# Performance work log

Measured on AMD Instinct MI355X. Metric: run time of the kernel, lower is better.

## Reference

```python
import jax, jax.numpy as jnp
import numpy as np

B, S, HID = 1, 2048, 2048   # batch, block_size, hidden_dim
H, D = 16, 128              # num_heads, head_dim
WORLD_SIZE = 4
LOCAL_BLOCK_IDX = 3         # last rank: all kv blocks are causally visible


def setup_inputs() -> dict:
    key = jax.random.key(0)
    ks = jax.random.split(key, 5)
    w = lambda k: jax.random.normal(k, (H * D, HID), dtype=jnp.float32) * 0.02
    return {
        "hidden_states": jax.random.normal(ks[0], (B, S, HID), dtype=jnp.float32),
        "q_w": w(ks[1]), "q_b": jnp.zeros((H * D,), jnp.float32),
        "k_w": w(ks[2]), "k_b": jnp.zeros((H * D,), jnp.float32),
        "v_w": w(ks[3]), "v_b": jnp.zeros((H * D,), jnp.float32),
        "o_w": jax.random.normal(ks[4], (HID, H * D), dtype=jnp.float32) * 0.02,
        "o_b": jnp.zeros((HID,), jnp.float32),
        "world_size": WORLD_SIZE,
        "local_block_idx": LOCAL_BLOCK_IDX,
    }


def reference(hidden_states, q_w, q_b, k_w, k_b, v_w, v_b, o_w, o_b,
              world_size, local_block_idx):
    Bsz, Sq, _ = hidden_states.shape

    def proj(w, b):  # (B,S,HID) -> (B,H,S,D)
        return (hidden_states @ w.T + b).reshape(Bsz, Sq, H, D).transpose(0, 2, 1, 3)

    q, k, v = proj(q_w, q_b), proj(k_w, k_b), proj(v_w, v_b)
    scale = D ** -0.5

    # ring_send_recv is a local copy, so K/V are identical every ring step;
    # only the causal masking differs (triu mask on the diagonal block step).
    scores_base = jnp.einsum('bhqd,bhkd->bhqk', q, k) * scale
    tri = jnp.triu(jnp.ones((Sq, Sq), bool), k=1)
    scores_diag = jnp.where(tri, -jnp.inf, scores_base)

    out = jnp.zeros((Bsz, H, Sq, D), hidden_states.dtype)
    mx = jnp.full((Bsz, H, Sq, 1), -jnp.inf, hidden_states.dtype)
    se = jnp.zeros((Bsz, H, Sq, 1), hidden_states.dtype)

    for step in range(world_size):  # small fixed ring loop
        kv_idx = (local_block_idx - step) % world_size
        scores = scores_diag if kv_idx == local_block_idx else scores_base
        # OnlineSoftmax.update (faithful, including block-wise normalization)
        bm = scores.max(axis=-1, keepdims=True)
        nm = jnp.maximum(mx, bm)
        old_s = jnp.exp(mx - nm)
        new_s = jnp.exp(bm - nm)
        be = jnp.exp(scores - bm)
        bs = be.sum(axis=-1, keepdims=True)
        se = se * old_s + bs * new_s
        aw = be / (bs + 1e-8)
        bo = jnp.einsum('bhqk,bhkd->bhqd', aw, v)
        out = out * old_s + bo * new_s
        mx = nm

    out = out / (se + 1e-8)  # OnlineSoftmax.finalize
    out = out.transpose(0, 2, 1, 3).reshape(Bsz, Sq, H * D)
    return out @ o_w.T + o_b
```

## Files before the change

kernel.cpp:

```cpp
#include <hip/hip_runtime.h>
#include <hip/hip_bf16.h>
#include <stdint.h>
#include <stddef.h>


typedef __attribute__((ext_vector_type(8))) short bf16x8;
typedef __attribute__((ext_vector_type(4))) float f32x4;

#define MFMA_BF16(a, b, c) __builtin_amdgcn_mfma_f32_16x16x32_bf16((a), (b), (c), 0, 0, 0)

__device__ __forceinline__ void load16_lds(const void* g, void* l) {
  __builtin_amdgcn_global_load_lds((const __attribute__((address_space(1))) void*)g,
                                   (__attribute__((address_space(3))) void*)l,
                                   16, 0, 0);
}

__device__ __forceinline__ unsigned short f2bf(float x) {
  union { __hip_bfloat16 b; unsigned short u; } cv;
  cv.b = __float2bfloat16(x);
  return cv.u;
}

__global__ __launch_bounds__(256) void cvt_all(
    const float4* __restrict__ s0, const float4* __restrict__ s1,
    const float4* __restrict__ s2, const float4* __restrict__ s3,
    const float4* __restrict__ s4,
    ushort4* __restrict__ d0, ushort4* __restrict__ d1,
    ushort4* __restrict__ d2, ushort4* __restrict__ d3,
    ushort4* __restrict__ d4) {
  const int seg = blockIdx.x >> 12;
  const int i = ((blockIdx.x & 4095) << 8) + threadIdx.x;
  const float4* s = seg == 0 ? s0 : seg == 1 ? s1 : seg == 2 ? s2 : seg == 3 ? s3 : s4;
  ushort4* d = seg == 0 ? d0 : seg == 1 ? d1 : seg == 2 ? d2 : seg == 3 ? d3 : d4;
  float4 v = s[i];
  ushort4 o;
  o.x = f2bf(v.x); o.y = f2bf(v.y); o.z = f2bf(v.z); o.w = f2bf(v.w);
  d[i] = o;
}

__global__ __launch_bounds__(256) void gemm_qkv(
    const unsigned short* __restrict__ A, const unsigned short* __restrict__ Bt,
    const float* __restrict__ qb, const float* __restrict__ kb,
    const float* __restrict__ vb,
    unsigned short* __restrict__ Qo, unsigned short* __restrict__ Ko,
    unsigned short* __restrict__ Vt) {
  __shared__ __align__(16) unsigned short sA[128 * 64];
  __shared__ __align__(16) unsigned short sB[128 * 64];
  const int tid = threadIdx.x;
  const int wave = tid >> 6, lane = tid & 63;
  const int quad = lane >> 4, l16 = lane & 15;
  const int wr = wave >> 1, wc = wave & 1;
  const int m0 = blockIdx.y << 7, n0 = blockIdx.x << 7;

  f32x4 acc[4][4] = {};

  for (int k0 = 0; k0 < 2048; k0 += 64) {
    __syncthreads();
#pragma unroll
    for (int t = 0; t < 4; t++) {
      const int i = t * 4 + wave;
      const int idx = i * 64 + lane;
      const int row = idx >> 3;
      const int c = (idx & 7) ^ (row & 7);
      load16_lds(A + (size_t)(m0 + row) * 2048 + k0 + c * 8, &sA[i * 512]);
      load16_lds(Bt + (size_t)(n0 + row) * 2048 + k0 + c * 8, &sB[i * 512]);
    }
    __syncthreads();
#pragma unroll
    for (int ks = 0; ks < 2; ks++) {
      bf16x8 af[4], bfr[4];
#pragma unroll
      for (int i = 0; i < 4; i++) {
        const int cs = ((ks * 4 + quad) ^ (l16 & 7)) << 3;
        af[i] = *(const bf16x8*)&sA[(wr * 64 + i * 16 + l16) * 64 + cs];
        bfr[i] = *(const bf16x8*)&sB[(wc * 64 + i * 16 + l16) * 64 + cs];
      }
#pragma unroll
      for (int mi = 0; mi < 4; mi++)
#pragma unroll
        for (int ni = 0; ni < 4; ni++)
          acc[mi][ni] = MFMA_BF16(af[mi], bfr[ni], acc[mi][ni]);
    }
  }

  const float qscale = 0.088388347648318447f * 1.4426950408889634f;
#pragma unroll
  for (int mi = 0; mi < 4; mi++) {
    const int row = m0 + wr * 64 + mi * 16 + quad * 4;
#pragma unroll
    for (int ni = 0; ni < 4; ni++) {
      const int col = n0 + wc * 64 + ni * 16 + l16;
#pragma unroll
      for (int r = 0; r < 4; r++) {
        const float v = acc[mi][ni][r];
        const int rr = row + r;
        if (col < 2048) {
          const int hh = col >> 7, d = col & 127;
          Qo[((size_t)hh * 2048 + rr) * 128 + d] = f2bf((v + qb[col]) * qscale);
        } else if (col < 4096) {
          const int f = col - 2048;
          const int hh = f >> 7, d = f & 127;
          Ko[((size_t)hh * 2048 + rr) * 128 + d] = f2bf(v + kb[f]);
        } else {
          const int f = col - 4096;
          const int hh = f >> 7, d = f & 127;
          Vt[((size_t)hh * 128 + d) * 2048 + rr] = f2bf(v + vb[f]);
        }
      }
    }
  }
}

__global__ __launch_bounds__(256, 2) void attn_fwd(
    const unsigned short* __restrict__ Q, const unsigned short* __restrict__ K,
    const unsigned short* __restrict__ V,
    unsigned short* __restrict__ O,
    const int* __restrict__ wsp) {
  const int qt = blockIdx.x, h = blockIdx.y;
  const int tid = threadIdx.x;
  const int wave = tid >> 6, lane = tid & 63;
  const int quad = lane >> 4, l16 = lane & 15;

  __shared__ __align__(16) unsigned short sK0[64 * 128];
  __shared__ __align__(16) unsigned short sK1[64 * 128];
  __shared__ __align__(16) unsigned short sV0[128 * 64];
  __shared__ __align__(16) unsigned short sV1[128 * 64];
  __shared__ __align__(16) unsigned short sP[4][16 * 64];

  const unsigned short* Qh = Q + (size_t)h * 2048 * 128;
  const unsigned short* Kh = K + (size_t)h * 2048 * 128;
  const unsigned short* Vh = V + (size_t)h * 128 * 2048;
  unsigned short* sPw = sP[wave];

  for (int c = wave; c < 16; c += 4) {
    const int rowc = lane >> 4;
    const int row = c * 4 + rowc;
    const int blk = (lane & 15) ^ (row & 15);
    load16_lds(Qh + (size_t)(qt * 64 + row) * 128 + blk * 8, &sK0[c * 512]);
  }
  __syncthreads();

  bf16x8 qf[4];
#pragma unroll
  for (int ds = 0; ds < 4; ds++)
    qf[ds] = *(const bf16x8*)&sK0[(wave * 16 + l16) * 128 + (((ds * 4 + quad) ^ l16) << 3)];
  __syncthreads();

  float m1 = -3.0e38f, l1 = 0.f, m2 = -3.0e38f, l2 = 0.f;
  f32x4 o1[8], o2[8];
#pragma unroll
  for (int j = 0; j < 8; j++) { o1[j] = f32x4{0.f, 0.f, 0.f, 0.f}; o2[j] = f32x4{0.f, 0.f, 0.f, 0.f}; }

  auto stageKV = [&](int kt, unsigned short* kDst, unsigned short* vDst) {
    const int k0 = kt << 6;
    for (int c = wave; c < 16; c += 4) {
      {
        const int rowc = lane >> 4;
        const int row = c * 4 + rowc;
        const int blk = (lane & 15) ^ (row & 15);
        load16_lds(Kh + (size_t)(k0 + row) * 128 + blk * 8, &kDst[c * 512]);
      }
      {
        const int rowc = lane >> 3;
        const int row = c * 8 + rowc;
        const int blk = (lane & 7) ^ (rowc & 7);
        load16_lds(Vh + (size_t)row * 2048 + k0 + blk * 8, &vDst[c * 512]);
      }
    }
  };

  auto softmax_update = [&](float& m, float& l, f32x4 (&o)[8],
                            const f32x4 (&stt)[4], bool masked, int k0) {
    const int qg = qt * 64 + wave * 16 + l16;
    float t[4][4];
    float mx = -3.0e38f;
#pragma unroll
    for (int ni = 0; ni < 4; ni++)
#pragma unroll
      for (int r = 0; r < 4; r++) {
        float v = stt[ni][r];
        if (masked && (k0 + ni * 16 + quad * 4 + r > qg)) v = -3.0e38f;
        t[ni][r] = v;
        mx = fmaxf(mx, v);
      }
    mx = fmaxf(mx, __shfl_xor(mx, 16));
    mx = fmaxf(mx, __shfl_xor(mx, 32));
    const float mn = fmaxf(m, mx);
    const float al = exp2f(m - mn);
    float rs = 0.f;
#pragma unroll
    for (int ni = 0; ni < 4; ni++) {
      union { unsigned short u[4]; uint2 v; } pk;
#pragma unroll
      for (int r = 0; r < 4; r++) {
        const float p = exp2f(t[ni][r] - mn);
        rs += p;
        pk.u[r] = f2bf(p);
      }
      const int off =
          l16 * 64 + (((ni * 2 + (quad >> 1)) ^ (l16 & 7)) << 3) + ((quad & 1) << 2);
      *(uint2*)&sPw[off] = pk.v;
    }
    rs += __shfl_xor(rs, 16);
    rs += __shfl_xor(rs, 32);
    const bool grew = !__all(mn == m);
    l = l * al + rs;
    m = mn;
    if (grew) {
#pragma unroll
      for (int r = 0; r < 4; r++) {
        const int src = (lane & 48) + quad * 4 + r;
        const float ab = __shfl(al, src);
#pragma unroll
        for (int j = 0; j < 8; j++) o[j][r] *= ab;
      }
    }
  };

  auto pv = [&](f32x4 (&o)[8], const unsigned short* vBuf) {
#pragma unroll
    for (int ks = 0; ks < 2; ks++) {
      const int cs = (((ks * 4 + quad) ^ (l16 & 7)) << 3);
      const bf16x8 pf = *(const bf16x8*)&sPw[l16 * 64 + cs];
#pragma unroll
      for (int j = 0; j < 8; j++) {
        const bf16x8 vf = *(const bf16x8*)&vBuf[(j * 16 + l16) * 64 + cs];
        o[j] = MFMA_BF16(pf, vf, o[j]);
      }
    }
  };

  auto compute_tile = [&](int kt, const unsigned short* kBuf,
                          const unsigned short* vBuf) {
    const int k0 = kt << 6;
    f32x4 st[4];
#pragma unroll
    for (int ni = 0; ni < 4; ni++) st[ni] = f32x4{0.f, 0.f, 0.f, 0.f};
#pragma unroll
    for (int ds = 0; ds < 4; ds++) {
#pragma unroll
      for (int ni = 0; ni < 4; ni++) {
        const bf16x8 kf =
            *(const bf16x8*)&kBuf[(ni * 16 + l16) * 128 + (((ds * 4 + quad) ^ l16) << 3)];
        st[ni] = MFMA_BF16(kf, qf[ds], st[ni]);
      }
    }

    if (kt == qt) {
      m1 = m2; l1 = l2;
#pragma unroll
      for (int j = 0; j < 8; j++) o1[j] = o2[j];
      softmax_update(m1, l1, o1, st, true, k0);
      pv(o1, vBuf);
    }
    softmax_update(m2, l2, o2, st, false, k0);
    pv(o2, vBuf);
  };

  stageKV(0, sK0, sV0);
  for (int kt2 = 0; kt2 < 32; kt2 += 2) {
    __syncthreads();
    if (kt2 + 1 < 32) stageKV(kt2 + 1, sK1, sV1);
    compute_tile(kt2, sK0, sV0);
    __syncthreads();
    if (kt2 + 2 < 32) stageKV(kt2 + 2, sK0, sV0);
    compute_tile(kt2 + 1, sK1, sV1);
  }

  const float fws = (float)(wsp[0] - 1);
  const float a = exp2f(m1 - m2);
  const float se = l1 * a + fws * l2;
  const float inv = 1.0f / (se + 1e-8f);
  const float f1 = (a / (l1 + 1e-8f)) * inv;
  const float f2 = (fws / (l2 + 1e-8f)) * inv;
#pragma unroll
  for (int r = 0; r < 4; r++) {
    const int src = (lane & 48) + quad * 4 + r;
    const float f1b = __shfl(f1, src);
    const float f2b = __shfl(f2, src);
    const int row = qt * 64 + wave * 16 + quad * 4 + r;
#pragma unroll
    for (int j = 0; j < 8; j++) {
      const float ov = o1[j][r] * f1b + o2[j][r] * f2b;
      O[(size_t)row * 2048 + h * 128 + j * 16 + l16] = f2bf(ov);
    }
  }
}

__global__ __launch_bounds__(256) void gemm_o(
    const unsigned short* __restrict__ A, const unsigned short* __restrict__ Bt,
    const float* __restrict__ ob, float* __restrict__ Cout) {
  __shared__ __align__(16) unsigned short sA[64 * 128];
  __shared__ __align__(16) unsigned short sB[128 * 128];
  const int tid = threadIdx.x;
  const int wave = tid >> 6, lane = tid & 63;
  const int quad = lane >> 4, l16 = lane & 15;
  const int wm = wave >> 1, wn = wave & 1;
  const int m0 = blockIdx.y << 6, n0 = blockIdx.x << 7;

  f32x4 acc[2][4] = {};

  for (int k0 = 0; k0 < 2048; k0 += 128) {
    __syncthreads();
#pragma unroll
    for (int t = 0; t < 4; t++) {
      const int i = t * 4 + wave;
      const int idx = i * 64 + lane;
      const int row = idx >> 4;
      const int c = (idx & 15) ^ (row & 15);
      load16_lds(A + (size_t)(m0 + row) * 2048 + k0 + c * 8, &sA[i * 512]);
    }
#pragma unroll
    for (int t = 0; t < 8; t++) {
      const int i = t * 4 + wave;
      const int idx = i * 64 + lane;
      const int row = idx >> 4;
      const int c = (idx & 15) ^ (row & 15);
      load16_lds(Bt + (size_t)(n0 + row) * 2048 + k0 + c * 8, &sB[i * 512]);
    }
    __syncthreads();
#pragma unroll
    for (int ks = 0; ks < 4; ks++) {
      const int cs = ((ks * 4 + quad) ^ l16) << 3;
      bf16x8 af[2], bfr[4];
#pragma unroll
      for (int i = 0; i < 2; i++)
        af[i] = *(const bf16x8*)&sA[(wm * 32 + i * 16 + l16) * 128 + cs];
#pragma unroll
      for (int i = 0; i < 4; i++)
        bfr[i] = *(const bf16x8*)&sB[(wn * 64 + i * 16 + l16) * 128 + cs];
#pragma unroll
      for (int mi = 0; mi < 2; mi++)
#pragma unroll
        for (int ni = 0; ni < 4; ni++)
          acc[mi][ni] = MFMA_BF16(af[mi], bfr[ni], acc[mi][ni]);
    }
  }

#pragma unroll
  for (int mi = 0; mi < 2; mi++) {
    const int row = m0 + wm * 32 + mi * 16 + quad * 4;
#pragma unroll
    for (int ni = 0; ni < 4; ni++) {
      const int col = n0 + wn * 64 + ni * 16 + l16;
#pragma unroll
      for (int r = 0; r < 4; r++) {
        Cout[(size_t)(row + r) * 2048 + col] = acc[mi][ni][r] + ob[col];
      }
    }
  }
}

extern "C" void kernel_launch(void* const* d_in, const int* in_sizes, int n_in,
                              void* d_out, int out_size, void* d_ws, size_t ws_size,
                              hipStream_t stream) {
  (void)in_sizes; (void)n_in; (void)out_size; (void)ws_size;
  const float* hs = (const float*)d_in[0];
  const float* qw = (const float*)d_in[1];
  const float* qb = (const float*)d_in[2];
  const float* kw = (const float*)d_in[3];
  const float* kb = (const float*)d_in[4];
  const float* vw = (const float*)d_in[5];
  const float* vb = (const float*)d_in[6];
  const float* ow = (const float*)d_in[7];
  const float* ob = (const float*)d_in[8];
  const int* wsz = (const int*)d_in[9];

  char* w = (char*)d_ws;
  unsigned short* hsb  = (unsigned short*)(w + 0);
  unsigned short* wqkv = (unsigned short*)(w + 8388608);
  unsigned short* owb  = (unsigned short*)(w + 33554432);
  unsigned short* Qb_  = (unsigned short*)(w + 41943040);
  unsigned short* Kb_  = (unsigned short*)(w + 50331648);
  unsigned short* Vtb  = (unsigned short*)(w + 58720256);
  unsigned short* atb  = (unsigned short*)(w + 67108864);

  cvt_all<<<20480, 256, 0, stream>>>(
      (const float4*)hs, (const float4*)qw, (const float4*)kw, (const float4*)vw,
      (const float4*)ow,
      (ushort4*)hsb, (ushort4*)wqkv, (ushort4*)(wqkv + 4194304),
      (ushort4*)(wqkv + 8388608), (ushort4*)owb);

  gemm_qkv<<<dim3(48, 16), 256, 0, stream>>>(hsb, wqkv, qb, kb, vb, Qb_, Kb_, Vtb);
  attn_fwd<<<dim3(32, 16), 256, 0, stream>>>(Qb_, Kb_, Vtb, atb, wsz);
  gemm_o<<<dim3(16, 32), 256, 0, stream>>>(atb, owb, ob, (float*)d_out);
}
```

Measured before the change: 322.0 us.

## Rewrite QKV GEMM with 256x256 tiles and double-buffered LDS pipeline

The QKV projection GEMM moves from 128x128 tiles with 4 waves to 256x256 tiles with 8 waves, and stages K-slices into double-buffered LDS so the next tile's global loads overlap the current MFMAs. Each K step is split into four phases with explicit barriers, vmcnt waits and setprio raised around the MFMA bursts. The aim is more reuse per LDS load and hiding load latency behind compute. In exchange the grid shrinks to 192 blocks, which is below the MI355X's 256 CUs, and the kernel uses more registers and LDS per block.

```diff
diff --git a/kernel.cpp b/kernel.cpp
--- a/kernel.cpp
+++ b/kernel.cpp
@@ -38,55 +38,85 @@
   d[i] = o;
 }
 
-__global__ __launch_bounds__(256) void gemm_qkv(
+__global__ __launch_bounds__(512, 2) void gemm_qkv(
     const unsigned short* __restrict__ A, const unsigned short* __restrict__ Bt,
     const float* __restrict__ qb, const float* __restrict__ kb,
     const float* __restrict__ vb,
     unsigned short* __restrict__ Qo, unsigned short* __restrict__ Ko,
     unsigned short* __restrict__ Vt) {
-  __shared__ __align__(16) unsigned short sA[128 * 64];
-  __shared__ __align__(16) unsigned short sB[128 * 64];
+  __shared__ __align__(16) unsigned short sA[2][2][256 * 32];
+  __shared__ __align__(16) unsigned short sB[2][2][256 * 32];
   const int tid = threadIdx.x;
   const int wave = tid >> 6, lane = tid & 63;
   const int quad = lane >> 4, l16 = lane & 15;
-  const int wr = wave >> 1, wc = wave & 1;
-  const int m0 = blockIdx.y << 7, n0 = blockIdx.x << 7;
-
-  f32x4 acc[4][4] = {};
-
-  for (int k0 = 0; k0 < 2048; k0 += 64) {
-    __syncthreads();
-#pragma unroll
-    for (int t = 0; t < 4; t++) {
-      const int i = t * 4 + wave;
-      const int idx = i * 64 + lane;
-      const int row = idx >> 3;
-      const int c = (idx & 7) ^ (row & 7);
-      load16_lds(A + (size_t)(m0 + row) * 2048 + k0 + c * 8, &sA[i * 512]);
-      load16_lds(Bt + (size_t)(n0 + row) * 2048 + k0 + c * 8, &sB[i * 512]);
-    }
-    __syncthreads();
-#pragma unroll
-    for (int ks = 0; ks < 2; ks++) {
-      bf16x8 af[4], bfr[4];
-#pragma unroll
-      for (int i = 0; i < 4; i++) {
-        const int cs = ((ks * 4 + quad) ^ (l16 & 7)) << 3;
-        af[i] = *(const bf16x8*)&sA[(wr * 64 + i * 16 + l16) * 64 + cs];
-        bfr[i] = *(const bf16x8*)&sB[(wc * 64 + i * 16 + l16) * 64 + cs];
-      }
-#pragma unroll
-      for (int mi = 0; mi < 4; mi++)
-#pragma unroll
-        for (int ni = 0; ni < 4; ni++)
-          acc[mi][ni] = MFMA_BF16(af[mi], bfr[ni], acc[mi][ni]);
-    }
-  }
+  const int wr = wave >> 2, wc = wave & 3;
+  const int m0 = blockIdx.y << 8, n0 = blockIdx.x << 8;
+
+  f32x4 acc[8][4] = {};
+  bf16x8 af[8], bf01[2], bf23[2];
+
+  const int srow = wave * 16 + (lane >> 2);
+  const int scol = (lane & 3) * 8;
+
+  auto stageA = [&](int kt_, int ks_) {
+    unsigned short* dst = &sA[kt_ & 1][ks_][0];
+    const unsigned short* src =
+        A + (size_t)(m0 + srow) * 2048 + kt_ * 64 + ks_ * 32 + scol;
+#pragma unroll
+    for (int rr = 0; rr < 2; rr++)
+      load16_lds(src + (size_t)rr * 128 * 2048, dst + (rr * 128 + wave * 16) * 32);
+  };
+  auto stageB = [&](int kt_, int ks_) {
+    unsigned short* dst = &sB[kt_ & 1][ks_][0];
+    const unsigned short* src =
+        Bt + (size_t)(n0 + srow) * 2048 + kt_ * 64 + ks_ * 32 + scol;
+#pragma unroll
+    for (int rr = 0; rr < 2; rr++)
+      load16_lds(src + (size_t)rr * 128 * 2048, dst + (rr * 128 + wave * 16) * 32);
+  };
+
+#define PHASE(KS, NB, BF, READ_A, STAGE_STMT, VM_STMT)                         \
+  {                                                                            \
+    const unsigned short* sAp = &sA[kt & 1][KS][0];                            \
+    const unsigned short* sBp = &sB[kt & 1][KS][0];                            \
+    if (READ_A) {                                                              \
+      _Pragma("unroll") for (int mi = 0; mi < 8; mi++)                         \
+          af[mi] = *(const bf16x8*)&sAp[(wr * 128 + mi * 16 + l16) * 32 + quad * 8]; \
+    }                                                                          \
+    _Pragma("unroll") for (int j = 0; j < 2; j++)                              \
+        BF[j] = *(const bf16x8*)&sBp[(wc * 64 + (NB + j) * 16 + l16) * 32 + quad * 8]; \
+    STAGE_STMT;                                                                \
+    __builtin_amdgcn_s_barrier();                                              \
+    asm volatile("s_waitcnt lgkmcnt(0)" ::: "memory");                         \
+    __builtin_amdgcn_s_setprio(1);                                             \
+    _Pragma("unroll") for (int mi = 0; mi < 8; mi++) {                         \
+      acc[mi][NB] = MFMA_BF16(af[mi], BF[0], acc[mi][NB]);                     \
+      acc[mi][NB + 1] = MFMA_BF16(af[mi], BF[1], acc[mi][NB + 1]);             \
+    }                                                                          \
+    __builtin_amdgcn_s_setprio(0);                                             \
+    VM_STMT;                                                                   \
+    __builtin_amdgcn_s_barrier();                                              \
+  }
+
+  stageA(0, 0); stageB(0, 0); stageA(0, 1); stageB(0, 1);
+  asm volatile("s_waitcnt vmcnt(4)" ::: "memory");
+  __builtin_amdgcn_s_barrier();
+
+  for (int kt = 0; kt < 32; kt++) {
+    const bool pf = (kt < 31);
+    PHASE(0, 0, bf01, true,  { if (pf) stageA(kt + 1, 0); }, {});
+    PHASE(0, 2, bf23, false, { if (pf) stageB(kt + 1, 0); },
+          { asm volatile("s_waitcnt vmcnt(4)" ::: "memory"); });
+    PHASE(1, 0, bf01, true,  { if (pf) stageA(kt + 1, 1); }, {});
+    PHASE(1, 2, bf23, false, { if (pf) stageB(kt + 1, 1); },
+          { asm volatile("s_waitcnt vmcnt(4)" ::: "memory"); });
+  }
+#undef PHASE
 
   const float qscale = 0.088388347648318447f * 1.4426950408889634f;
 #pragma unroll
-  for (int mi = 0; mi < 4; mi++) {
-    const int row = m0 + wr * 64 + mi * 16 + quad * 4;
+  for (int mi = 0; mi < 8; mi++) {
+    const int row = m0 + wr * 128 + mi * 16 + quad * 4;
 #pragma unroll
     for (int ni = 0; ni < 4; ni++) {
       const int col = n0 + wc * 64 + ni * 16 + l16;
@@ -381,7 +411,7 @@
       (ushort4*)hsb, (ushort4*)wqkv, (ushort4*)(wqkv + 4194304),
       (ushort4*)(wqkv + 8388608), (ushort4*)owb);
 
-  gemm_qkv<<<dim3(48, 16), 256, 0, stream>>>(hsb, wqkv, qb, kb, vb, Qb_, Kb_, Vtb);
+  gemm_qkv<<<dim3(24, 8), 512, 0, stream>>>(hsb, wqkv, qb, kb, vb, Qb_, Kb_, Vtb);
   attn_fwd<<<dim3(32, 16), 256, 0, stream>>>(Qb_, Kb_, Vtb, atb, wsz);
   gemm_o<<<dim3(16, 32), 256, 0, stream>>>(atb, owb, ob, (float*)d_out);
 }
```

Result: no change. 320.2 us (-0.6%).
